# Kernel tuning notes

Hardware: AMD Instinct MI355X
Metric: run time of the kernel (lower is better)

## Reference

```python
import jax, jax.numpy as jnp
import numpy as np
from jax import lax

HIDDEN = 16
DN = ('NCHW', 'OIHW', 'NCHW')

def setup_inputs() -> dict:
    key = jax.random.key(0)
    k1, k2, k3 = jax.random.split(key, 3)
    b, t, c, h, w = 8, 12, 5, 256, 256
    x = jax.random.normal(k1, (b, t, c, h, w), dtype=jnp.float32)
    # PyTorch-like init scale for conv weights
    W_cell = jax.random.normal(k2, (4 * HIDDEN, c + HIDDEN, 3, 3), dtype=jnp.float32) * 0.05
    b_cell = jnp.zeros((4 * HIDDEN,), dtype=jnp.float32)
    W_final = jax.random.normal(k3, (1, HIDDEN, 1, 1), dtype=jnp.float32) * 0.1
    b_final = jnp.zeros((1,), dtype=jnp.float32)
    return {"x": x, "W_cell": W_cell, "b_cell": b_cell,
            "W_final": W_final, "b_final": b_final}

def _cell_step(h_c, x_t, W_cell, b_cell):
    h_cur, c_cur = h_c
    combined = jnp.concatenate([x_t, h_cur], axis=1)          # [B, C+H, H, W]
    conv = lax.conv_general_dilated(combined, W_cell, (1, 1), 'SAME',
                                    dimension_numbers=DN)
    conv = conv + b_cell[None, :, None, None]                  # [B, 4H, H, W]
    cc_i, cc_f, cc_o, cc_g = jnp.split(conv, 4, axis=1)
    i = jax.nn.sigmoid(cc_i)
    f = jax.nn.sigmoid(cc_f)
    o = jax.nn.sigmoid(cc_o)
    g = jnp.tanh(cc_g)
    c_next = f * c_cur + i * g
    h_next = o * jnp.tanh(c_next)
    return h_next, c_next

def reference(x, W_cell, b_cell, W_final, b_final):
    b, t, c, hh, ww = x.shape
    h0 = jnp.zeros((b, HIDDEN, hh, ww), dtype=x.dtype)
    c0 = jnp.zeros((b, HIDDEN, hh, ww), dtype=x.dtype)
    xt = jnp.moveaxis(x, 1, 0)  # [T, B, C, H, W] for scan over time

    def step(carry, x_t):
        return _cell_step(carry, x_t, W_cell, b_cell), None

    (h_last, _), _ = lax.scan(step, (h0, c0), xt)
    out = lax.conv_general_dilated(h_last, W_final, (1, 1), 'SAME',
                                   dimension_numbers=DN)
    out = out + b_final[None, :, None, None]
    return out
```

## Files before the change

### kernel.cpp

```cpp
#include <hip/hip_runtime.h>
#include <math.h>

#define HIDDEN 16
#define CIN 5
#define BB 8
#define TT 12
#define HH 256
#define WW 256
#define KPAD 32
#define TX 32
#define TY 8
#define HALO_X 34
#define HALO_Y 10
#define NPX (HALO_X * HALO_Y)

typedef __attribute__((ext_vector_type(8))) short bf16x8;
typedef __attribute__((ext_vector_type(4))) float floatx4;

__device__ __forceinline__ unsigned short f2bf(float f) {
    unsigned int u = __float_as_uint(f);
    u += 0x7fffu + ((u >> 16) & 1u);
    return (unsigned short)(u >> 16);
}
__device__ __forceinline__ float bf2f(unsigned short s) {
    return __uint_as_float(((unsigned int)s) << 16);
}
__device__ __forceinline__ float fast_sigmoid(float x) { return 1.0f / (1.0f + __expf(-x)); }
__device__ __forceinline__ float fast_tanh(float x) {
    float e2 = __expf(-2.0f * fabsf(x));
    float t = (1.0f - e2) / (1.0f + e2);
    return copysignf(t, x);
}

__global__ void prep_kernel(const float* __restrict__ Wc,
                            unsigned short* __restrict__ Wfrag) {
    int i = blockIdx.x * 256 + threadIdx.x;
    if (i >= 9 * 4 * 64 * 8) return;
    int j    = i & 7;
    int lane = (i >> 3) & 63;
    int g    = (i >> 9) & 3;
    int tap  = i >> 11;
    int k    = ((lane >> 4) << 3) + j;
    int col  = lane & 15;
    int o    = g * 16 + col;
    float w  = 0.0f;
    if (k < 21) {
        int ci_ref = (k < 16) ? (5 + k) : (k - 16);
        w = Wc[(o * 21 + ci_ref) * 9 + tap];
    }
    Wfrag[i] = f2bf(w);
}

__global__ __launch_bounds__(256)
void convlstm_step_kernel(const float* __restrict__ x, int t,
                          const unsigned short* __restrict__ h_in,
                          unsigned short* __restrict__ h_out,
                          float* __restrict__ c_state,
                          const unsigned short* __restrict__ Wfrag,
                          const float* __restrict__ bias,
                          int first) {
    __shared__ unsigned short tile[NPX * KPAD];

    const int tid  = threadIdx.x;
    const int lane = tid & 63;
    const int wave = tid >> 6;
    const int x0 = blockIdx.x * TX;
    const int y0 = blockIdx.y * TY;
    const int bb = blockIdx.z;

    for (int i = tid; i < NPX; i += 256) {
        int ly = i / HALO_X;
        int lx = i - ly * HALO_X;
        int gy = y0 + ly - 1;
        int gx = x0 + lx - 1;
        bool inb = (gy >= 0 && gy < HH && gx >= 0 && gx < WW);
        unsigned short* row = &tile[i * KPAD];
        if (inb && !first) {
            size_t hb = ((size_t)bb * HH * WW + (size_t)gy * WW + gx) * HIDDEN;
            *(uint4*)&row[0] = *(const uint4*)&h_in[hb];
            *(uint4*)&row[8] = *(const uint4*)&h_in[hb + 8];
        } else {
            uint4 z = {0, 0, 0, 0};
            *(uint4*)&row[0] = z;
            *(uint4*)&row[8] = z;
        }
        #pragma unroll
        for (int ci = 0; ci < CIN; ++ci) {
            float v = 0.0f;
            if (inb) v = x[(((size_t)bb * TT + t) * CIN + ci) * (size_t)(HH * WW)
                           + (size_t)gy * WW + gx];
            row[16 + ci] = f2bf(v);
        }
        row[21] = 0; row[22] = 0; row[23] = 0;
        uint4 z2 = {0, 0, 0, 0};
        *(uint4*)&row[24] = z2;
    }
    __syncthreads();

    const int u    = lane & 15;
    const int quad = lane >> 4;

    float bg[4];
    #pragma unroll
    for (int g = 0; g < 4; ++g) bg[g] = bias[g * 16 + u];

    floatx4 acc[4][4];
    #pragma unroll
    for (int ml = 0; ml < 4; ++ml)
        #pragma unroll
        for (int g = 0; g < 4; ++g)
            acc[ml][g] = (floatx4){bg[g], bg[g], bg[g], bg[g]};

    #pragma unroll 1
    for (int tap = 0; tap < 9; ++tap) {
        int ky = tap / 3;
        int kx = tap - ky * 3;
        bf16x8 bfr[4];
        #pragma unroll
        for (int g = 0; g < 4; ++g)
            bfr[g] = *(const bf16x8*)&Wfrag[(size_t)((tap * 4 + g) * 64 + lane) * 8];
        #pragma unroll
        for (int ml = 0; ml < 4; ++ml) {
            int m  = wave + ml * 4;
            int my = m >> 1;
            int mx = (m & 1) << 4;
            int yt = my + ky;
            int xt = mx + u + kx;
            bf16x8 af = *(const bf16x8*)&tile[(yt * HALO_X + xt) * KPAD + quad * 8];
            #pragma unroll
            for (int g = 0; g < 4; ++g)
                acc[ml][g] = __builtin_amdgcn_mfma_f32_16x16x32_bf16(
                    af, bfr[g], acc[ml][g], 0, 0, 0);
        }
    }

    #pragma unroll
    for (int ml = 0; ml < 4; ++ml) {
        int m  = wave + ml * 4;
        int my = m >> 1;
        int mx = (m & 1) << 4;
        int py = y0 + my;
        #pragma unroll
        for (int r = 0; r < 4; ++r) {
            int pxx = x0 + mx + quad * 4 + r;
            size_t idx = ((size_t)bb * HH * WW + (size_t)py * WW + pxx) * HIDDEN + u;
            float ig = fast_sigmoid(acc[ml][0][r]);
            float fg = fast_sigmoid(acc[ml][1][r]);
            float og = fast_sigmoid(acc[ml][2][r]);
            float gg = fast_tanh(acc[ml][3][r]);
            float c_old = first ? 0.0f : c_state[idx];
            float c_new = fg * c_old + ig * gg;
            c_state[idx] = c_new;
            h_out[idx] = f2bf(og * fast_tanh(c_new));
        }
    }
}

__global__ void final_conv_kernel(const unsigned short* __restrict__ h,
                                  const float* __restrict__ Wf,
                                  const float* __restrict__ bf_,
                                  float* __restrict__ out) {
    int i = blockIdx.x * 256 + threadIdx.x;
    if (i >= BB * HH * WW) return;
    size_t base = (size_t)i * HIDDEN;
    uint4 v0 = *(const uint4*)&h[base];
    uint4 v1 = *(const uint4*)&h[base + 8];
    const unsigned short* p0 = (const unsigned short*)&v0;
    const unsigned short* p1 = (const unsigned short*)&v1;
    float s = bf_[0];
    #pragma unroll
    for (int k = 0; k < 8; ++k) s += Wf[k] * bf2f(p0[k]);
    #pragma unroll
    for (int k = 0; k < 8; ++k) s += Wf[8 + k] * bf2f(p1[k]);
    out[i] = s;
}

extern "C" void kernel_launch(void* const* d_in, const int* in_sizes, int n_in,
                              void* d_out, int out_size, void* d_ws, size_t ws_size,
                              hipStream_t stream) {
    const float* x  = (const float*)d_in[0];
    const float* Wc = (const float*)d_in[1];
    const float* bc = (const float*)d_in[2];
    const float* Wf = (const float*)d_in[3];
    const float* bf = (const float*)d_in[4];
    float* out = (float*)d_out;

    char* ws = (char*)d_ws;
    const size_t h_bytes = (size_t)BB * HH * WW * HIDDEN * 2;
    const size_t c_bytes = (size_t)BB * HH * WW * HIDDEN * 4;
    unsigned short* h_a = (unsigned short*)(ws);
    unsigned short* h_b = (unsigned short*)(ws + h_bytes);
    float* c            = (float*)(ws + 2 * h_bytes);
    unsigned short* Wfr = (unsigned short*)(ws + 2 * h_bytes + c_bytes);

    prep_kernel<<<(9 * 4 * 64 * 8 + 255) / 256, 256, 0, stream>>>(Wc, Wfr);

    dim3 grid(WW / TX, HH / TY, BB);
    dim3 block(256, 1, 1);

    const unsigned short* h_in = h_a;
    for (int t = 0; t < TT; ++t) {
        unsigned short* h_out = (t & 1) ? h_b : h_a;
        convlstm_step_kernel<<<grid, block, 0, stream>>>(
            x, t, h_in, h_out, c, Wfr, bc, (t == 0) ? 1 : 0);
        h_in = h_out;
    }

    final_conv_kernel<<<(BB * HH * WW + 255) / 256, 256, 0, stream>>>(
        h_in, Wf, bf, out);
}
```

Baseline: 781.4 us.

## Pre-pack input frames to bf16 channel-last, pad LDS stride, split accumulators for occupancy

Adds a prepass that converts all input frames to a packed bf16 pixel-major layout with 8 channels per pixel. Each step can then load the x halo with one 16-byte read instead of five strided fp32 loads. The LDS row stride is padded from 32 to 40 elements to reduce bank conflicts on the fragment reads. The M-tiles are processed in two halves with fewer live accumulators, under launch bounds requesting 5 blocks per CU, to raise occupancy. The costs are an extra full pass over x, larger LDS per block, and a workspace-size dependency: the packed path is used only when the workspace is large enough.

```diff
diff --git a/kernel.cpp b/kernel.cpp
--- a/kernel.cpp
+++ b/kernel.cpp
@@ -7,12 +7,12 @@
 #define TT 12
 #define HH 256
 #define WW 256
-#define KPAD 32
 #define TX 32
 #define TY 8
 #define HALO_X 34
 #define HALO_Y 10
 #define NPX (HALO_X * HALO_Y)
+#define STRIDE 40
 
 typedef __attribute__((ext_vector_type(8))) short bf16x8;
 typedef __attribute__((ext_vector_type(4))) float floatx4;
@@ -32,8 +32,8 @@
     return copysignf(t, x);
 }
 
-__global__ void prep_kernel(const float* __restrict__ Wc,
-                            unsigned short* __restrict__ Wfrag) {
+__global__ void prep_w_kernel(const float* __restrict__ Wc,
+                              unsigned short* __restrict__ Wfrag) {
     int i = blockIdx.x * 256 + threadIdx.x;
     if (i >= 9 * 4 * 64 * 8) return;
     int j    = i & 7;
@@ -51,15 +51,31 @@
     Wfrag[i] = f2bf(w);
 }
 
-__global__ __launch_bounds__(256)
+__global__ void prep_x_kernel(const float* __restrict__ x,
+                              unsigned short* __restrict__ xp) {
+    size_t n = (size_t)blockIdx.x * 256 + threadIdx.x;
+    const size_t TOTPX = (size_t)BB * TT * HH * WW;
+    if (n >= TOTPX) return;
+    size_t bt  = n / (size_t)(HH * WW);
+    size_t pix = n - bt * (size_t)(HH * WW);
+    const float* src = x + bt * (size_t)CIN * HH * WW + pix;
+    unsigned short v[8];
+    #pragma unroll
+    for (int c = 0; c < CIN; ++c) v[c] = f2bf(src[(size_t)c * HH * WW]);
+    v[5] = 0; v[6] = 0; v[7] = 0;
+    *(uint4*)&xp[n * 8] = *(const uint4*)v;
+}
+
+__global__ __launch_bounds__(256, 5)
 void convlstm_step_kernel(const float* __restrict__ x, int t,
+                          const unsigned short* __restrict__ xp,
                           const unsigned short* __restrict__ h_in,
                           unsigned short* __restrict__ h_out,
                           float* __restrict__ c_state,
                           const unsigned short* __restrict__ Wfrag,
                           const float* __restrict__ bias,
-                          int first) {
-    __shared__ unsigned short tile[NPX * KPAD];
+                          int first, int use_xp) {
+    __shared__ unsigned short tile[NPX * STRIDE];
 
     const int tid  = threadIdx.x;
     const int lane = tid & 63;
@@ -74,26 +90,35 @@
         int gy = y0 + ly - 1;
         int gx = x0 + lx - 1;
         bool inb = (gy >= 0 && gy < HH && gx >= 0 && gx < WW);
-        unsigned short* row = &tile[i * KPAD];
+        unsigned short* row = &tile[i * STRIDE];
+        uint4 z = {0, 0, 0, 0};
         if (inb && !first) {
             size_t hb = ((size_t)bb * HH * WW + (size_t)gy * WW + gx) * HIDDEN;
             *(uint4*)&row[0] = *(const uint4*)&h_in[hb];
             *(uint4*)&row[8] = *(const uint4*)&h_in[hb + 8];
         } else {
-            uint4 z = {0, 0, 0, 0};
             *(uint4*)&row[0] = z;
             *(uint4*)&row[8] = z;
         }
-        #pragma unroll
-        for (int ci = 0; ci < CIN; ++ci) {
-            float v = 0.0f;
-            if (inb) v = x[(((size_t)bb * TT + t) * CIN + ci) * (size_t)(HH * WW)
-                           + (size_t)gy * WW + gx];
-            row[16 + ci] = f2bf(v);
-        }
-        row[21] = 0; row[22] = 0; row[23] = 0;
-        uint4 z2 = {0, 0, 0, 0};
-        *(uint4*)&row[24] = z2;
+        if (use_xp) {
+            if (inb) {
+                size_t xb = (((size_t)bb * TT + t) * (size_t)(HH * WW)
+                             + (size_t)gy * WW + gx) * 8;
+                *(uint4*)&row[16] = *(const uint4*)&xp[xb];
+            } else {
+                *(uint4*)&row[16] = z;
+            }
+        } else {
+            #pragma unroll
+            for (int ci = 0; ci < CIN; ++ci) {
+                float v = 0.0f;
+                if (inb) v = x[(((size_t)bb * TT + t) * CIN + ci) * (size_t)(HH * WW)
+                               + (size_t)gy * WW + gx];
+                row[16 + ci] = f2bf(v);
+            }
+            row[21] = 0; row[22] = 0; row[23] = 0;
+        }
+        *(uint4*)&row[24] = z;
     }
     __syncthreads();
 
@@ -104,54 +129,61 @@
     #pragma unroll
     for (int g = 0; g < 4; ++g) bg[g] = bias[g * 16 + u];
 
-    floatx4 acc[4][4];
-    #pragma unroll
-    for (int ml = 0; ml < 4; ++ml)
+    #pragma unroll 1
+    for (int half = 0; half < 2; ++half) {
+        floatx4 acc[2][4];
+        int abase[2];
         #pragma unroll
-        for (int g = 0; g < 4; ++g)
-            acc[ml][g] = (floatx4){bg[g], bg[g], bg[g], bg[g]};
-
-    #pragma unroll 1
-    for (int tap = 0; tap < 9; ++tap) {
-        int ky = tap / 3;
-        int kx = tap - ky * 3;
-        bf16x8 bfr[4];
-        #pragma unroll
-        for (int g = 0; g < 4; ++g)
-            bfr[g] = *(const bf16x8*)&Wfrag[(size_t)((tap * 4 + g) * 64 + lane) * 8];
-        #pragma unroll
-        for (int ml = 0; ml < 4; ++ml) {
+        for (int mh = 0; mh < 2; ++mh) {
+            int ml = half * 2 + mh;
             int m  = wave + ml * 4;
             int my = m >> 1;
             int mx = (m & 1) << 4;
-            int yt = my + ky;
-            int xt = mx + u + kx;
-            bf16x8 af = *(const bf16x8*)&tile[(yt * HALO_X + xt) * KPAD + quad * 8];
+            abase[mh] = (my * HALO_X + mx + u) * STRIDE + quad * 8;
             #pragma unroll
             for (int g = 0; g < 4; ++g)
-                acc[ml][g] = __builtin_amdgcn_mfma_f32_16x16x32_bf16(
-                    af, bfr[g], acc[ml][g], 0, 0, 0);
-        }
-    }
-
-    #pragma unroll
-    for (int ml = 0; ml < 4; ++ml) {
-        int m  = wave + ml * 4;
-        int my = m >> 1;
-        int mx = (m & 1) << 4;
-        int py = y0 + my;
+                acc[mh][g] = (floatx4){bg[g], bg[g], bg[g], bg[g]};
+        }
+
+        #pragma unroll 3
+        for (int tap = 0; tap < 9; ++tap) {
+            int ky = tap / 3;
+            int kx = tap - ky * 3;
+            int toff = (ky * HALO_X + kx) * STRIDE;
+            bf16x8 bfr[4];
+            #pragma unroll
+            for (int g = 0; g < 4; ++g)
+                bfr[g] = *(const bf16x8*)&Wfrag[(size_t)((tap * 4 + g) * 64 + lane) * 8];
+            #pragma unroll
+            for (int mh = 0; mh < 2; ++mh) {
+                bf16x8 af = *(const bf16x8*)&tile[abase[mh] + toff];
+                #pragma unroll
+                for (int g = 0; g < 4; ++g)
+                    acc[mh][g] = __builtin_amdgcn_mfma_f32_16x16x32_bf16(
+                        af, bfr[g], acc[mh][g], 0, 0, 0);
+            }
+        }
+
         #pragma unroll
-        for (int r = 0; r < 4; ++r) {
-            int pxx = x0 + mx + quad * 4 + r;
-            size_t idx = ((size_t)bb * HH * WW + (size_t)py * WW + pxx) * HIDDEN + u;
-            float ig = fast_sigmoid(acc[ml][0][r]);
-            float fg = fast_sigmoid(acc[ml][1][r]);
-            float og = fast_sigmoid(acc[ml][2][r]);
-            float gg = fast_tanh(acc[ml][3][r]);
-            float c_old = first ? 0.0f : c_state[idx];
-            float c_new = fg * c_old + ig * gg;
-            c_state[idx] = c_new;
-            h_out[idx] = f2bf(og * fast_tanh(c_new));
+        for (int mh = 0; mh < 2; ++mh) {
+            int ml = half * 2 + mh;
+            int m  = wave + ml * 4;
+            int my = m >> 1;
+            int mx = (m & 1) << 4;
+            int py = y0 + my;
+            #pragma unroll
+            for (int r = 0; r < 4; ++r) {
+                int pxx = x0 + mx + quad * 4 + r;
+                size_t idx = ((size_t)bb * HH * WW + (size_t)py * WW + pxx) * HIDDEN + u;
+                float ig = fast_sigmoid(acc[mh][0][r]);
+                float fg = fast_sigmoid(acc[mh][1][r]);
+                float og = fast_sigmoid(acc[mh][2][r]);
+                float gg = fast_tanh(acc[mh][3][r]);
+                float c_old = first ? 0.0f : c_state[idx];
+                float c_new = fg * c_old + ig * gg;
+                c_state[idx] = c_new;
+                h_out[idx] = f2bf(og * fast_tanh(c_new));
+            }
         }
     }
 }
@@ -188,12 +220,23 @@
     char* ws = (char*)d_ws;
     const size_t h_bytes = (size_t)BB * HH * WW * HIDDEN * 2;
     const size_t c_bytes = (size_t)BB * HH * WW * HIDDEN * 4;
+    const size_t w_bytes = 9 * 4 * 64 * 8 * 2;
+    const size_t x_bytes = (size_t)BB * TT * HH * WW * 8 * 2;
+
     unsigned short* h_a = (unsigned short*)(ws);
     unsigned short* h_b = (unsigned short*)(ws + h_bytes);
     float* c            = (float*)(ws + 2 * h_bytes);
     unsigned short* Wfr = (unsigned short*)(ws + 2 * h_bytes + c_bytes);
-
-    prep_kernel<<<(9 * 4 * 64 * 8 + 255) / 256, 256, 0, stream>>>(Wc, Wfr);
+    unsigned short* xp  = (unsigned short*)(ws + 2 * h_bytes + c_bytes + w_bytes);
+
+    const int use_xp =
+        (ws_size >= 2 * h_bytes + c_bytes + w_bytes + x_bytes) ? 1 : 0;
+
+    prep_w_kernel<<<(9 * 4 * 64 * 8 + 255) / 256, 256, 0, stream>>>(Wc, Wfr);
+    if (use_xp) {
+        size_t totpx = (size_t)BB * TT * HH * WW;
+        prep_x_kernel<<<(int)((totpx + 255) / 256), 256, 0, stream>>>(x, xp);
+    }
 
     dim3 grid(WW / TX, HH / TY, BB);
     dim3 block(256, 1, 1);
@@ -202,7 +245,8 @@
     for (int t = 0; t < TT; ++t) {
         unsigned short* h_out = (t & 1) ? h_b : h_a;
         convlstm_step_kernel<<<grid, block, 0, stream>>>(
-            x, t, h_in, h_out, c, Wfr, bc, (t == 0) ? 1 : 0);
+            x, t, use_xp ? xp : (const unsigned short*)0,
+            h_in, h_out, c, Wfr, bc, (t == 0) ? 1 : 0, use_xp);
         h_in = h_out;
     }
 
```

Result: faster. 691.1 us (-11.6%).
